# Kernel tuning notes

Hardware: AMD Instinct MI355X
Metric: run time of the kernel (lower is better)

The kernel has to match this reference:

```python
import jax, jax.numpy as jnp
import numpy as np

D = 4096
B = 8192
LN_EPS = 1e-5


def setup_inputs() -> dict:
    key = jax.random.key(0)
    k1, k2, k3 = jax.random.split(key, 3)
    x = jax.random.normal(k1, (B, D), dtype=jnp.float32)
    x0 = jax.random.normal(k2, (B, D), dtype=jnp.float32)
    # xavier_normal_ on (D, 1): std = sqrt(2 / (D + 1))
    weight = jax.random.normal(k3, (D,), dtype=jnp.float32) * np.float32(np.sqrt(2.0 / (D + 1)))
    bias = jnp.zeros((D,), dtype=jnp.float32)
    gamma = jnp.ones((D,), dtype=jnp.float32)   # LayerNorm weight
    beta = jnp.zeros((D,), dtype=jnp.float32)   # LayerNorm bias
    return {"x": x, "x0": x0, "weight": weight, "bias": bias, "gamma": gamma, "beta": beta}


def reference(x, x0, weight, bias, gamma, beta):
    # torch: (x[:,:,None] @ x0[:,None,:]) @ weight  ==  x * (x0 @ weight)
    # weighted[b,i] = sum_j x[b,i] * x0[b,j] * w[j] = x[b,i] * (x0[b] . w)
    scale = x0 @ weight                      # (B,)  per-batch scalar
    pre = x * scale[:, None] + bias + x      # scale + bias + residual, (B, D)
    # LayerNorm over last dim
    mean = jnp.mean(pre, axis=-1, keepdims=True)
    var = jnp.mean(jnp.square(pre - mean), axis=-1, keepdims=True)
    out = (pre - mean) * jax.lax.rsqrt(var + LN_EPS) * gamma + beta
    # dropout is identity at inference
    return out
```

## Files before the change

### kernel.cpp

```cpp
#include <hip/hip_runtime.h>

#define DIM 4096
#define LN_EPS 1e-5f
#define NTHREADS 512
#define VPT 2
#define NWAVES (NTHREADS / 64)

typedef float vfloat4 __attribute__((ext_vector_type(4)));

__global__ __launch_bounds__(NTHREADS) void crosslayer_ln_kernel(
    const float* __restrict__ x,
    const float* __restrict__ x0,
    const float* __restrict__ w,
    const float* __restrict__ bias,
    const float* __restrict__ gamma,
    const float* __restrict__ beta,
    float* __restrict__ out)
{
    const int row = blockIdx.x;
    const int tid = threadIdx.x;
    const int wave = tid >> 6;
    const int lane = tid & 63;

    const float4* __restrict__ x0v = reinterpret_cast<const float4*>(x0 + (size_t)row * DIM);
    const float4* __restrict__ xv  = reinterpret_cast<const float4*>(x  + (size_t)row * DIM);
    const float4* __restrict__ wv  = reinterpret_cast<const float4*>(w);
    const float4* __restrict__ bv  = reinterpret_cast<const float4*>(bias);
    const float4* __restrict__ gv  = reinterpret_cast<const float4*>(gamma);
    const float4* __restrict__ btv = reinterpret_cast<const float4*>(beta);
    vfloat4* __restrict__ ov = reinterpret_cast<vfloat4*>(out + (size_t)row * DIM);

    const int i0 = tid;
    const int i1 = NTHREADS + tid;

    const float4 a0 = x0v[i0];
    const float4 a1 = x0v[i1];
    const float4 w0 = wv[i0];
    const float4 w1 = wv[i1];
    const float4 xA = xv[i0];
    const float4 xB = xv[i1];
    const float4 bA = bv[i0];
    const float4 bB = bv[i1];

    float dot = a0.x*w0.x + a0.y*w0.y + a0.z*w0.z + a0.w*w0.w
              + a1.x*w1.x + a1.y*w1.y + a1.z*w1.z + a1.w*w1.w;
    float Sx  = xA.x + xA.y + xA.z + xA.w + xB.x + xB.y + xB.z + xB.w;
    float Sxx = xA.x*xA.x + xA.y*xA.y + xA.z*xA.z + xA.w*xA.w
              + xB.x*xB.x + xB.y*xB.y + xB.z*xB.z + xB.w*xB.w;
    float Sxb = xA.x*bA.x + xA.y*bA.y + xA.z*bA.z + xA.w*bA.w
              + xB.x*bB.x + xB.y*bB.y + xB.z*bB.z + xB.w*bB.w;
    float Sb  = bA.x + bA.y + bA.z + bA.w + bB.x + bB.y + bB.z + bB.w;
    float Sbb = bA.x*bA.x + bA.y*bA.y + bA.z*bA.z + bA.w*bA.w
              + bB.x*bB.x + bB.y*bB.y + bB.z*bB.z + bB.w*bB.w;

    const float4 gA  = gv[i0];
    const float4 gB  = gv[i1];
    const float4 btA = btv[i0];
    const float4 btB = btv[i1];

    #pragma unroll
    for (int o = 1; o < 64; o <<= 1) {
        dot += __shfl_xor(dot, o, 64);
        Sx  += __shfl_xor(Sx,  o, 64);
        Sxx += __shfl_xor(Sxx, o, 64);
        Sxb += __shfl_xor(Sxb, o, 64);
        Sb  += __shfl_xor(Sb,  o, 64);
        Sbb += __shfl_xor(Sbb, o, 64);
    }

    __shared__ float red[6][NWAVES];
    if (lane == 0) {
        red[0][wave] = dot; red[1][wave] = Sx;  red[2][wave] = Sxx;
        red[3][wave] = Sxb; red[4][wave] = Sb;  red[5][wave] = Sbb;
    }
    __syncthreads();

    float tdot = 0.f, tSx = 0.f, tSxx = 0.f, tSxb = 0.f, tSb = 0.f, tSbb = 0.f;
    #pragma unroll
    for (int i = 0; i < NWAVES; ++i) {
        tdot += red[0][i]; tSx  += red[1][i]; tSxx += red[2][i];
        tSxb += red[3][i]; tSb  += red[4][i]; tSbb += red[5][i];
    }

    const float m    = 1.f + tdot;
    const float mean = (m * tSx + tSb) * (1.f / DIM);
    const float Ex2  = (m * m * tSxx + 2.f * m * tSxb + tSbb) * (1.f / DIM);
    const float var  = Ex2 - mean * mean;
    const float inv  = rsqrtf(var + LN_EPS);

    vfloat4 o0, o1;
    o0.x = fmaf((fmaf(m, xA.x, bA.x) - mean) * inv, gA.x, btA.x);
    o0.y = fmaf((fmaf(m, xA.y, bA.y) - mean) * inv, gA.y, btA.y);
    o0.z = fmaf((fmaf(m, xA.z, bA.z) - mean) * inv, gA.z, btA.z);
    o0.w = fmaf((fmaf(m, xA.w, bA.w) - mean) * inv, gA.w, btA.w);
    o1.x = fmaf((fmaf(m, xB.x, bB.x) - mean) * inv, gB.x, btB.x);
    o1.y = fmaf((fmaf(m, xB.y, bB.y) - mean) * inv, gB.y, btB.y);
    o1.z = fmaf((fmaf(m, xB.z, bB.z) - mean) * inv, gB.z, btB.z);
    o1.w = fmaf((fmaf(m, xB.w, bB.w) - mean) * inv, gB.w, btB.w);
    __builtin_nontemporal_store(o0, &ov[i0]);
    __builtin_nontemporal_store(o1, &ov[i1]);
}

extern "C" void kernel_launch(void* const* d_in, const int* in_sizes, int n_in,
                              void* d_out, int out_size, void* d_ws, size_t ws_size,
                              hipStream_t stream) {
    const float* x     = (const float*)d_in[0];
    const float* x0    = (const float*)d_in[1];
    const float* w     = (const float*)d_in[2];
    const float* bias  = (const float*)d_in[3];
    const float* gamma = (const float*)d_in[4];
    const float* beta  = (const float*)d_in[5];
    float* out = (float*)d_out;

    const int B = in_sizes[0] / DIM;
    crosslayer_ln_kernel<<<B, NTHREADS, 0, stream>>>(x, x0, w, bias, gamma, beta, out);
}
```

Measured before the change: 63.61 us.

## Process eight rows per block and cache LayerNorm params in shared memory

Each block now handles eight consecutive rows, loading the weight and bias vectors into registers and gamma/beta into LDS once per block instead of once per row. The mean and variance are computed from the materialized pre-norm values in a second reduction, replacing the single-pass moment expansion. This cuts redundant parameter reads but serializes rows within a block and adds an extra barrier per row, reducing concurrent memory requests.

```diff
diff --git a/kernel.cpp b/kernel.cpp
--- a/kernel.cpp
+++ b/kernel.cpp
@@ -2,13 +2,13 @@
 
 #define DIM 4096
 #define LN_EPS 1e-5f
-#define NTHREADS 512
-#define VPT 2
-#define NWAVES (NTHREADS / 64)
+#define NT 512
+#define RPB 8
+#define NWAVES (NT / 64)
 
 typedef float vfloat4 __attribute__((ext_vector_type(4)));
 
-__global__ __launch_bounds__(NTHREADS) void crosslayer_ln_kernel(
+__global__ __launch_bounds__(NT) void crosslayer_ln_kernel(
     const float* __restrict__ x,
     const float* __restrict__ x0,
     const float* __restrict__ w,
@@ -17,88 +17,97 @@
     const float* __restrict__ beta,
     float* __restrict__ out)
 {
-    const int row = blockIdx.x;
-    const int tid = threadIdx.x;
+    const int tid  = threadIdx.x;
     const int wave = tid >> 6;
     const int lane = tid & 63;
+    const int i0 = tid;
+    const int i1 = NT + tid;
 
-    const float4* __restrict__ x0v = reinterpret_cast<const float4*>(x0 + (size_t)row * DIM);
-    const float4* __restrict__ xv  = reinterpret_cast<const float4*>(x  + (size_t)row * DIM);
+    __shared__ float4 sg[DIM / 4];
+    __shared__ float4 sbt[DIM / 4];
+    __shared__ float dred[2][NWAVES];
+    __shared__ float2 mred[2][NWAVES];
+
     const float4* __restrict__ wv  = reinterpret_cast<const float4*>(w);
     const float4* __restrict__ bv  = reinterpret_cast<const float4*>(bias);
     const float4* __restrict__ gv  = reinterpret_cast<const float4*>(gamma);
     const float4* __restrict__ btv = reinterpret_cast<const float4*>(beta);
-    vfloat4* __restrict__ ov = reinterpret_cast<vfloat4*>(out + (size_t)row * DIM);
 
-    const int i0 = tid;
-    const int i1 = NTHREADS + tid;
-
-    const float4 a0 = x0v[i0];
-    const float4 a1 = x0v[i1];
+    sg[i0]  = gv[i0];
+    sg[i1]  = gv[i1];
+    sbt[i0] = btv[i0];
+    sbt[i1] = btv[i1];
     const float4 w0 = wv[i0];
     const float4 w1 = wv[i1];
-    const float4 xA = xv[i0];
-    const float4 xB = xv[i1];
-    const float4 bA = bv[i0];
-    const float4 bB = bv[i1];
-
-    float dot = a0.x*w0.x + a0.y*w0.y + a0.z*w0.z + a0.w*w0.w
-              + a1.x*w1.x + a1.y*w1.y + a1.z*w1.z + a1.w*w1.w;
-    float Sx  = xA.x + xA.y + xA.z + xA.w + xB.x + xB.y + xB.z + xB.w;
-    float Sxx = xA.x*xA.x + xA.y*xA.y + xA.z*xA.z + xA.w*xA.w
-              + xB.x*xB.x + xB.y*xB.y + xB.z*xB.z + xB.w*xB.w;
-    float Sxb = xA.x*bA.x + xA.y*bA.y + xA.z*bA.z + xA.w*bA.w
-              + xB.x*bB.x + xB.y*bB.y + xB.z*bB.z + xB.w*bB.w;
-    float Sb  = bA.x + bA.y + bA.z + bA.w + bB.x + bB.y + bB.z + bB.w;
-    float Sbb = bA.x*bA.x + bA.y*bA.y + bA.z*bA.z + bA.w*bA.w
-              + bB.x*bB.x + bB.y*bB.y + bB.z*bB.z + bB.w*bB.w;
-
-    const float4 gA  = gv[i0];
-    const float4 gB  = gv[i1];
-    const float4 btA = btv[i0];
-    const float4 btB = btv[i1];
-
-    #pragma unroll
-    for (int o = 1; o < 64; o <<= 1) {
-        dot += __shfl_xor(dot, o, 64);
-        Sx  += __shfl_xor(Sx,  o, 64);
-        Sxx += __shfl_xor(Sxx, o, 64);
-        Sxb += __shfl_xor(Sxb, o, 64);
-        Sb  += __shfl_xor(Sb,  o, 64);
-        Sbb += __shfl_xor(Sbb, o, 64);
-    }
-
-    __shared__ float red[6][NWAVES];
-    if (lane == 0) {
-        red[0][wave] = dot; red[1][wave] = Sx;  red[2][wave] = Sxx;
-        red[3][wave] = Sxb; red[4][wave] = Sb;  red[5][wave] = Sbb;
-    }
+    const float4 b0 = bv[i0];
+    const float4 b1 = bv[i1];
     __syncthreads();
 
-    float tdot = 0.f, tSx = 0.f, tSxx = 0.f, tSxb = 0.f, tSb = 0.f, tSbb = 0.f;
-    #pragma unroll
-    for (int i = 0; i < NWAVES; ++i) {
-        tdot += red[0][i]; tSx  += red[1][i]; tSxx += red[2][i];
-        tSxb += red[3][i]; tSb  += red[4][i]; tSbb += red[5][i];
+    const size_t rowbase = (size_t)blockIdx.x * RPB;
+
+    for (int r = 0; r < RPB; ++r) {
+        const size_t row = rowbase + r;
+        const float4* __restrict__ x0v = reinterpret_cast<const float4*>(x0 + row * DIM);
+        const float4* __restrict__ xv  = reinterpret_cast<const float4*>(x  + row * DIM);
+        vfloat4* __restrict__ ov = reinterpret_cast<vfloat4*>(out + row * DIM);
+
+        const float4 a0 = x0v[i0];
+        const float4 a1 = x0v[i1];
+        const float4 xA = xv[i0];
+        const float4 xB = xv[i1];
+
+        float dot = a0.x*w0.x + a0.y*w0.y + a0.z*w0.z + a0.w*w0.w
+                  + a1.x*w1.x + a1.y*w1.y + a1.z*w1.z + a1.w*w1.w;
+        #pragma unroll
+        for (int o = 1; o < 64; o <<= 1) dot += __shfl_xor(dot, o, 64);
+        if (lane == 0) dred[r & 1][wave] = dot;
+        __syncthreads();
+        float td = 0.f;
+        #pragma unroll
+        for (int i = 0; i < NWAVES; ++i) td += dred[r & 1][i];
+        const float m = 1.f + td;
+
+        float pA0 = fmaf(m, xA.x, b0.x), pA1 = fmaf(m, xA.y, b0.y);
+        float pA2 = fmaf(m, xA.z, b0.z), pA3 = fmaf(m, xA.w, b0.w);
+        float pB0 = fmaf(m, xB.x, b1.x), pB1 = fmaf(m, xB.y, b1.y);
+        float pB2 = fmaf(m, xB.z, b1.z), pB3 = fmaf(m, xB.w, b1.w);
+
+        float sum   = pA0 + pA1 + pA2 + pA3 + pB0 + pB1 + pB2 + pB3;
+        float sumsq = pA0*pA0 + pA1*pA1 + pA2*pA2 + pA3*pA3
+                    + pB0*pB0 + pB1*pB1 + pB2*pB2 + pB3*pB3;
+        #pragma unroll
+        for (int o = 1; o < 64; o <<= 1) {
+            sum   += __shfl_xor(sum,   o, 64);
+            sumsq += __shfl_xor(sumsq, o, 64);
+        }
+        if (lane == 0) mred[r & 1][wave] = make_float2(sum, sumsq);
+        __syncthreads();
+        float tsum = 0.f, tsq = 0.f;
+        #pragma unroll
+        for (int i = 0; i < NWAVES; ++i) {
+            const float2 v = mred[r & 1][i];
+            tsum += v.x; tsq += v.y;
+        }
+        const float mean = tsum * (1.f / DIM);
+        const float var  = tsq * (1.f / DIM) - mean * mean;
+        const float inv  = rsqrtf(var + LN_EPS);
+
+        const float4 gA  = sg[i0];
+        const float4 gB  = sg[i1];
+        const float4 btA = sbt[i0];
+        const float4 btB = sbt[i1];
+        vfloat4 o0, o1;
+        o0.x = fmaf((pA0 - mean) * inv, gA.x, btA.x);
+        o0.y = fmaf((pA1 - mean) * inv, gA.y, btA.y);
+        o0.z = fmaf((pA2 - mean) * inv, gA.z, btA.z);
+        o0.w = fmaf((pA3 - mean) * inv, gA.w, btA.w);
+        o1.x = fmaf((pB0 - mean) * inv, gB.x, btB.x);
+        o1.y = fmaf((pB1 - mean) * inv, gB.y, btB.y);
+        o1.z = fmaf((pB2 - mean) * inv, gB.z, btB.z);
+        o1.w = fmaf((pB3 - mean) * inv, gB.w, btB.w);
+        __builtin_nontemporal_store(o0, &ov[i0]);
+        __builtin_nontemporal_store(o1, &ov[i1]);
     }
-
-    const float m    = 1.f + tdot;
-    const float mean = (m * tSx + tSb) * (1.f / DIM);
-    const float Ex2  = (m * m * tSxx + 2.f * m * tSxb + tSbb) * (1.f / DIM);
-    const float var  = Ex2 - mean * mean;
-    const float inv  = rsqrtf(var + LN_EPS);
-
-    vfloat4 o0, o1;
-    o0.x = fmaf((fmaf(m, xA.x, bA.x) - mean) * inv, gA.x, btA.x);
-    o0.y = fmaf((fmaf(m, xA.y, bA.y) - mean) * inv, gA.y, btA.y);
-    o0.z = fmaf((fmaf(m, xA.z, bA.z) - mean) * inv, gA.z, btA.z);
-    o0.w = fmaf((fmaf(m, xA.w, bA.w) - mean) * inv, gA.w, btA.w);
-    o1.x = fmaf((fmaf(m, xB.x, bB.x) - mean) * inv, gB.x, btB.x);
-    o1.y = fmaf((fmaf(m, xB.y, bB.y) - mean) * inv, gB.y, btB.y);
-    o1.z = fmaf((fmaf(m, xB.z, bB.z) - mean) * inv, gB.z, btB.z);
-    o1.w = fmaf((fmaf(m, xB.w, bB.w) - mean) * inv, gB.w, btB.w);
-    __builtin_nontemporal_store(o0, &ov[i0]);
-    __builtin_nontemporal_store(o1, &ov[i1]);
 }
 
 extern "C" void kernel_launch(void* const* d_in, const int* in_sizes, int n_in,
@@ -113,5 +122,6 @@
     float* out = (float*)d_out;
 
     const int B = in_sizes[0] / DIM;
-    crosslayer_ln_kernel<<<B, NTHREADS, 0, stream>>>(x, x0, w, bias, gamma, beta, out);
+    const int nblocks = B / RPB;
+    crosslayer_ln_kernel<<<nblocks, NT, 0, stream>>>(x, x0, w, bias, gamma, beta, out);
 }
```

Result: no change. 64.73 us (+1.8%).
